# Kernel optimization log

Measured on AMD Instinct MI355X. Metric: run time of the kernel, lower is better.

Reference implementation:

```python
import jax, jax.numpy as jnp
import numpy as np

N, F, H, C = 50000, 128, 4, 32  # nodes, in-features, heads, per-head dim
E = 800000
D = H * C  # concat output dim = 128


def _tconv(x, src, dst, ea, Wq, bq, Wk, bk, Wv, bv, We, Ws, bs):
    # PyG TransformerConv (concat=True, root_weight=True, beta=False, eval mode)
    n = x.shape[0]
    q = (x @ Wq + bq).reshape(n, H, C)
    k = (x @ Wk + bk).reshape(n, H, C)
    v = (x @ Wv + bv).reshape(n, H, C)
    e = (ea @ We).reshape(-1, H, C)            # edge embedding [E,H,C]
    kj = k[src] + e                            # gathered keys + edge emb
    alpha = jnp.einsum('ehc,ehc->eh', q[dst], kj) / jnp.sqrt(jnp.float32(C))
    amax = jax.ops.segment_max(alpha, dst, num_segments=n)
    ex = jnp.exp(alpha - amax[dst])
    denom = jax.ops.segment_sum(ex, dst, num_segments=n)
    w = ex / (denom[dst] + 1e-16)              # segment softmax over in-edges
    msg = (v[src] + e) * w[:, :, None]
    out = jax.ops.segment_sum(msg, dst, num_segments=n).reshape(n, D)
    return out + x @ Ws + bs                   # skip connection


def setup_inputs() -> dict:
    key = jax.random.key(0)
    ks = jax.random.split(key, 24)
    s = lambda i, shape, scale: jax.random.normal(ks[i], shape, dtype=jnp.float32) * scale
    inp = {
        'x': s(0, (N, F), 1.0),
        'edge_index': jax.random.randint(ks[1], (2, E), 0, N),
        'edge_attr': s(2, (E,), 1.0),
        # layer 1 (in = F)
        'Wq1': s(3, (F, D), 1.0 / np.sqrt(F)), 'bq1': jnp.zeros((D,), jnp.float32),
        'Wk1': s(4, (F, D), 1.0 / np.sqrt(F)), 'bk1': jnp.zeros((D,), jnp.float32),
        'Wv1': s(5, (F, D), 1.0 / np.sqrt(F)), 'bv1': jnp.zeros((D,), jnp.float32),
        'We1': s(6, (1, D), 1.0),
        'Ws1': s(7, (F, D), 1.0 / np.sqrt(F)), 'bs1': jnp.zeros((D,), jnp.float32),
        # layer 2 (in = D)
        'Wq2': s(8, (D, D), 1.0 / np.sqrt(D)), 'bq2': jnp.zeros((D,), jnp.float32),
        'Wk2': s(9, (D, D), 1.0 / np.sqrt(D)), 'bk2': jnp.zeros((D,), jnp.float32),
        'Wv2': s(10, (D, D), 1.0 / np.sqrt(D)), 'bv2': jnp.zeros((D,), jnp.float32),
        'We2': s(11, (1, D), 1.0),
        'Ws2': s(12, (D, D), 1.0 / np.sqrt(D)), 'bs2': jnp.zeros((D,), jnp.float32),
    }
    return inp


def reference(x, edge_index, edge_attr,
              Wq1, bq1, Wk1, bk1, Wv1, bv1, We1, Ws1, bs1,
              Wq2, bq2, Wk2, bk2, Wv2, bv2, We2, Ws2, bs2):
    src, dst = edge_index[0], edge_index[1]
    ea = edge_attr.reshape(-1, 1)
    h = _tconv(x, src, dst, ea, Wq1, bq1, Wk1, bk1, Wv1, bv1, We1, Ws1, bs1)
    h = jax.nn.relu(h)  # dropout is identity in eval mode
    h = _tconv(h, src, dst, ea, Wq2, bq2, Wk2, bk2, Wv2, bv2, We2, Ws2, bs2)
    return jax.nn.relu(h)
```

## Files before the change

### kernel.cpp

```cpp
#include <hip/hip_runtime.h>


#define TPB 256

typedef __attribute__((ext_vector_type(8))) short short8v;
typedef __attribute__((ext_vector_type(4))) float f32x4;

__device__ __forceinline__ unsigned short f2bf(float f) {
    unsigned u = __float_as_uint(f);
    u = (u + 0x7FFFu + ((u >> 16) & 1u)) >> 16;
    return (unsigned short)u;
}
__device__ __forceinline__ float bf2f(unsigned short s) {
    return __uint_as_float((unsigned)s << 16);
}
__device__ __forceinline__ float4 bf4_to_f4(ushort4 u) {
    return make_float4(bf2f(u.x), bf2f(u.y), bf2f(u.z), bf2f(u.w));
}

__global__ void __launch_bounds__(TPB) cvt_bf16_k(const float* __restrict__ in,
                                                  unsigned short* __restrict__ out,
                                                  int n4)
{
    int i = blockIdx.x * TPB + threadIdx.x;
    if (i >= n4) return;
    float4 v = *(const float4*)(in + (size_t)i * 4);
    ushort4 o;
    o.x = f2bf(v.x); o.y = f2bf(v.y); o.z = f2bf(v.z); o.w = f2bf(v.w);
    *(ushort4*)(out + (size_t)i * 4) = o;
}

__global__ void __launch_bounds__(TPB) prepack_k(
    const float* __restrict__ Wq, const float* __restrict__ Wk,
    const float* __restrict__ Wv, const float* __restrict__ Ws,
    unsigned short* __restrict__ pack)
{
    int i = blockIdx.x * TPB + threadIdx.x;
    int j = i & 7, l = (i >> 3) & 63, t = (i >> 9) & 3, c = (i >> 11) & 7, g = (i >> 14) & 3;
    const float* W = g == 0 ? Wq : (g == 1 ? Wk : (g == 2 ? Wv : Ws));
    int kk = t * 32 + (l >> 4) * 8 + j;
    int nn = c * 16 + (l & 15);
    pack[i] = f2bf(W[kk * 128 + nn]);
}

__global__ void __launch_bounds__(TPB) gemm_mfma_k(
    const unsigned short* __restrict__ A, int M,
    const unsigned short* __restrict__ pack,
    const float* __restrict__ bq, const float* __restrict__ bk,
    const float* __restrict__ bv, const float* __restrict__ bs,
    unsigned short* __restrict__ oq, unsigned short* __restrict__ ok,
    unsigned short* __restrict__ ov, float* __restrict__ os)
{
    const int g = blockIdx.y;
    const int row0 = blockIdx.x * 128;
    const int wv = threadIdx.x >> 6;
    const int lane = threadIdx.x & 63;
    const int rbase = row0 + wv * 32;
    const int rlo = lane & 15;
    const int kg = (lane >> 4) * 8;

    const short8v z8 = {0, 0, 0, 0, 0, 0, 0, 0};
    short8v a[2][4];
#pragma unroll
    for (int m = 0; m < 2; ++m) {
        int row = rbase + m * 16 + rlo;
#pragma unroll
        for (int t = 0; t < 4; ++t)
            a[m][t] = (row < M) ? *(const short8v*)(A + (size_t)row * 128 + t * 32 + kg)
                                : z8;
    }

    f32x4 acc[2][8];
#pragma unroll
    for (int m = 0; m < 2; ++m)
#pragma unroll
        for (int c = 0; c < 8; ++c)
            acc[m][c] = (f32x4){0.f, 0.f, 0.f, 0.f};

    const unsigned short* bp = pack + (size_t)g * (8 * 4 * 512);
#pragma unroll
    for (int c = 0; c < 8; ++c) {
        short8v b[4];
#pragma unroll
        for (int t = 0; t < 4; ++t)
            b[t] = *(const short8v*)(bp + (c * 4 + t) * 512 + lane * 8);
#pragma unroll
        for (int t = 0; t < 4; ++t) {
            acc[0][c] = __builtin_amdgcn_mfma_f32_16x16x32_bf16(a[0][t], b[t], acc[0][c], 0, 0, 0);
            acc[1][c] = __builtin_amdgcn_mfma_f32_16x16x32_bf16(a[1][t], b[t], acc[1][c], 0, 0, 0);
        }
    }

    const float* bias = g == 0 ? bq : (g == 1 ? bk : (g == 2 ? bv : bs));
    const int rof = (lane >> 4) * 4;
    if (g == 3) {
#pragma unroll
        for (int c = 0; c < 8; ++c) {
            float bb = bias[c * 16 + rlo];
#pragma unroll
            for (int m = 0; m < 2; ++m)
#pragma unroll
                for (int j = 0; j < 4; ++j) {
                    int row = rbase + m * 16 + rof + j;
                    if (row < M) os[(size_t)row * 128 + c * 16 + rlo] = acc[m][c][j] + bb;
                }
        }
    } else {
        unsigned short* out = g == 0 ? oq : (g == 1 ? ok : ov);
#pragma unroll
        for (int c = 0; c < 8; ++c) {
            float bb = bias[c * 16 + rlo];
#pragma unroll
            for (int m = 0; m < 2; ++m)
#pragma unroll
                for (int j = 0; j < 4; ++j) {
                    int row = rbase + m * 16 + rof + j;
                    if (row < M) out[(size_t)row * 128 + c * 16 + rlo] = f2bf(acc[m][c][j] + bb);
                }
        }
    }
}

__global__ void __launch_bounds__(TPB) hist_k(const int* __restrict__ dst,
                                              int* __restrict__ deg, int E)
{
    int e = blockIdx.x * TPB + threadIdx.x;
    if (e < E) atomicAdd(&deg[dst[e]], 1);
}

__global__ void __launch_bounds__(TPB) scan_a_k(const int* __restrict__ deg, int n,
                                                int* __restrict__ incl,
                                                int* __restrict__ bsum)
{
    __shared__ int ts[TPB];
    const int base = blockIdx.x * 1024;
    int vals[4], s = 0;
#pragma unroll
    for (int j = 0; j < 4; ++j) {
        int i = base + threadIdx.x * 4 + j;
        vals[j] = (i < n) ? deg[i] : 0;
        s += vals[j];
    }
    ts[threadIdx.x] = s;
    __syncthreads();
    for (int off = 1; off < TPB; off <<= 1) {
        int u = (threadIdx.x >= off) ? ts[threadIdx.x - off] : 0;
        __syncthreads();
        ts[threadIdx.x] += u;
        __syncthreads();
    }
    int run = ts[threadIdx.x] - s;
#pragma unroll
    for (int j = 0; j < 4; ++j) {
        run += vals[j];
        int i = base + threadIdx.x * 4 + j;
        if (i < n) incl[i] = run;
    }
    if (threadIdx.x == TPB - 1) bsum[blockIdx.x] = ts[TPB - 1];
}

__global__ void __launch_bounds__(TPB) scan_b_k(int* __restrict__ bsum, int nb)
{
    __shared__ int ts[TPB];
    int t = threadIdx.x;
    int v = (t < nb) ? bsum[t] : 0;
    ts[t] = v;
    __syncthreads();
    for (int off = 1; off < TPB; off <<= 1) {
        int u = (t >= off) ? ts[t - off] : 0;
        __syncthreads();
        ts[t] += u;
        __syncthreads();
    }
    if (t < nb) bsum[t] = ts[t] - v;
}

__global__ void __launch_bounds__(TPB) finalize_k(const int* __restrict__ incl,
                                                  const int* __restrict__ deg,
                                                  const int* __restrict__ bsum, int n,
                                                  int* __restrict__ row_ptr,
                                                  int* __restrict__ cursor)
{
    const int base = blockIdx.x * 1024;
    const int boff = bsum[blockIdx.x];
#pragma unroll
    for (int j = 0; j < 4; ++j) {
        int i = base + threadIdx.x * 4 + j;
        if (i < n) {
            int iv = incl[i] + boff;
            int st = iv - deg[i];
            row_ptr[i] = st;
            cursor[i] = st;
            if (i == n - 1) row_ptr[n] = iv;
        }
    }
}

__global__ void __launch_bounds__(TPB) scatter_k(
    const int* __restrict__ src, const int* __restrict__ dst,
    const float* __restrict__ ea, int* __restrict__ cursor,
    int* __restrict__ csr_src, float* __restrict__ csr_ea, int E)
{
    int e = blockIdx.x * TPB + threadIdx.x;
    if (e >= E) return;
    int pos = atomicAdd(&cursor[dst[e]], 1);
    csr_src[pos] = src[e];
    csr_ea[pos] = ea[e];
}

template <bool BF16OUT>
__global__ void __launch_bounds__(TPB) node_attn_k(
    const unsigned short* __restrict__ q, const unsigned short* __restrict__ k,
    const unsigned short* __restrict__ v, const float* __restrict__ skip,
    const float* __restrict__ We,
    const int* __restrict__ row_ptr, const int* __restrict__ csr_src,
    const float* __restrict__ csr_ea,
    void* __restrict__ outp, int n)
{
    const int node = blockIdx.x * 4 + (threadIdx.x >> 6);
    if (node >= n) return;
    const int lane = threadIdx.x & 63;
    const bool vside = lane >= 32;
    const int c4 = (lane & 31) * 4;
    const unsigned short* gbase = vside ? v : k;

    const float4 we4 = *(const float4*)(We + c4);
    const float4 qv = bf4_to_f4(*(const ushort4*)(q + (size_t)node * 128 + c4));
    const int p0 = row_ptr[node], p1 = row_ptr[node + 1];
    const float C = 0.17677669529663687f;

    float m = -3.4e38f, l = 0.f;
    float4 acc = make_float4(0.f, 0.f, 0.f, 0.f);

    for (int base = p0; base < p1; base += 64) {
        const int cnt = min(64, p1 - base);
        int sv = 0;
        float av = 0.f;
        if (lane < cnt) {
            sv = csr_src[base + lane];
            av = csr_ea[base + lane];
        }
        int j = 0;
        for (; j + 4 <= cnt; j += 4) {
            int s0 = __shfl(sv, j), s1 = __shfl(sv, j + 1);
            int s2 = __shfl(sv, j + 2), s3 = __shfl(sv, j + 3);
            float a0 = __shfl(av, j), a1 = __shfl(av, j + 1);
            float a2 = __shfl(av, j + 2), a3 = __shfl(av, j + 3);
            ushort4 u0 = *(const ushort4*)(gbase + (size_t)s0 * 128 + c4);
            ushort4 u1 = *(const ushort4*)(gbase + (size_t)s1 * 128 + c4);
            ushort4 u2 = *(const ushort4*)(gbase + (size_t)s2 * 128 + c4);
            ushort4 u3 = *(const ushort4*)(gbase + (size_t)s3 * 128 + c4);
            float4 f0 = bf4_to_f4(u0), f1 = bf4_to_f4(u1);
            float4 f2 = bf4_to_f4(u2), f3 = bf4_to_f4(u3);
            float4 e0, e1, e2, e3;
            e0.x = fmaf(a0, we4.x, f0.x); e0.y = fmaf(a0, we4.y, f0.y);
            e0.z = fmaf(a0, we4.z, f0.z); e0.w = fmaf(a0, we4.w, f0.w);
            e1.x = fmaf(a1, we4.x, f1.x); e1.y = fmaf(a1, we4.y, f1.y);
            e1.z = fmaf(a1, we4.z, f1.z); e1.w = fmaf(a1, we4.w, f1.w);
            e2.x = fmaf(a2, we4.x, f2.x); e2.y = fmaf(a2, we4.y, f2.y);
            e2.z = fmaf(a2, we4.z, f2.z); e2.w = fmaf(a2, we4.w, f2.w);
            e3.x = fmaf(a3, we4.x, f3.x); e3.y = fmaf(a3, we4.y, f3.y);
            e3.z = fmaf(a3, we4.z, f3.z); e3.w = fmaf(a3, we4.w, f3.w);
            float d0 = e0.x * qv.x + e0.y * qv.y + e0.z * qv.z + e0.w * qv.w;
            float d1 = e1.x * qv.x + e1.y * qv.y + e1.z * qv.z + e1.w * qv.w;
            float d2 = e2.x * qv.x + e2.y * qv.y + e2.z * qv.z + e2.w * qv.w;
            float d3 = e3.x * qv.x + e3.y * qv.y + e3.z * qv.z + e3.w * qv.w;
            d0 += __shfl_xor(d0, 1); d0 += __shfl_xor(d0, 2); d0 += __shfl_xor(d0, 4);
            d1 += __shfl_xor(d1, 1); d1 += __shfl_xor(d1, 2); d1 += __shfl_xor(d1, 4);
            d2 += __shfl_xor(d2, 1); d2 += __shfl_xor(d2, 2); d2 += __shfl_xor(d2, 4);
            d3 += __shfl_xor(d3, 1); d3 += __shfl_xor(d3, 2); d3 += __shfl_xor(d3, 4);
            float al0 = __shfl(d0, lane & 31) * C;
            float al1 = __shfl(d1, lane & 31) * C;
            float al2 = __shfl(d2, lane & 31) * C;
            float al3 = __shfl(d3, lane & 31) * C;
            float mn = fmax(m, fmax(fmax(al0, al1), fmax(al2, al3)));
            float sc = __expf(m - mn);
            float pe0 = __expf(al0 - mn), pe1 = __expf(al1 - mn);
            float pe2 = __expf(al2 - mn), pe3 = __expf(al3 - mn);
            l = fmaf(l, sc, (pe0 + pe1) + (pe2 + pe3));
            acc.x = fmaf(acc.x, sc, fmaf(pe0, e0.x, fmaf(pe1, e1.x, fmaf(pe2, e2.x, pe3 * e3.x))));
            acc.y = fmaf(acc.y, sc, fmaf(pe0, e0.y, fmaf(pe1, e1.y, fmaf(pe2, e2.y, pe3 * e3.y))));
            acc.z = fmaf(acc.z, sc, fmaf(pe0, e0.z, fmaf(pe1, e1.z, fmaf(pe2, e2.z, pe3 * e3.z))));
            acc.w = fmaf(acc.w, sc, fmaf(pe0, e0.w, fmaf(pe1, e1.w, fmaf(pe2, e2.w, pe3 * e3.w))));
            m = mn;
        }
        for (; j < cnt; ++j) {
            int s0 = __shfl(sv, j);
            float a0 = __shfl(av, j);
            ushort4 u0 = *(const ushort4*)(gbase + (size_t)s0 * 128 + c4);
            float4 f0 = bf4_to_f4(u0);
            float4 e0;
            e0.x = fmaf(a0, we4.x, f0.x); e0.y = fmaf(a0, we4.y, f0.y);
            e0.z = fmaf(a0, we4.z, f0.z); e0.w = fmaf(a0, we4.w, f0.w);
            float d0 = e0.x * qv.x + e0.y * qv.y + e0.z * qv.z + e0.w * qv.w;
            d0 += __shfl_xor(d0, 1); d0 += __shfl_xor(d0, 2); d0 += __shfl_xor(d0, 4);
            float al0 = __shfl(d0, lane & 31) * C;
            float mn = fmax(m, al0);
            float sc = __expf(m - mn);
            float pe0 = __expf(al0 - mn);
            l = fmaf(l, sc, pe0);
            acc.x = fmaf(acc.x, sc, pe0 * e0.x);
            acc.y = fmaf(acc.y, sc, pe0 * e0.y);
            acc.z = fmaf(acc.z, sc, pe0 * e0.z);
            acc.w = fmaf(acc.w, sc, pe0 * e0.w);
            m = mn;
        }
    }

    if (vside) {
        float inv = 1.f / (l + 1e-16f);
        float4 sk = *(const float4*)(skip + (size_t)node * 128 + c4);
        float o0 = fmaxf(fmaf(acc.x, inv, sk.x), 0.f);
        float o1 = fmaxf(fmaf(acc.y, inv, sk.y), 0.f);
        float o2 = fmaxf(fmaf(acc.z, inv, sk.z), 0.f);
        float o3 = fmaxf(fmaf(acc.w, inv, sk.w), 0.f);
        if (BF16OUT) {
            ushort4 o;
            o.x = f2bf(o0); o.y = f2bf(o1); o.z = f2bf(o2); o.w = f2bf(o3);
            *(ushort4*)((unsigned short*)outp + (size_t)node * 128 + c4) = o;
        } else {
            *(float4*)((float*)outp + (size_t)node * 128 + c4) =
                make_float4(o0, o1, o2, o3);
        }
    }
}

extern "C" void kernel_launch(void* const* d_in, const int* in_sizes, int n_in,
                              void* d_out, int out_size, void* d_ws, size_t ws_size,
                              hipStream_t stream)
{
    const float* x   = (const float*)d_in[0];
    const int*   ei  = (const int*)d_in[1];
    const float* ea  = (const float*)d_in[2];
    const float* Wq1 = (const float*)d_in[3];  const float* bq1 = (const float*)d_in[4];
    const float* Wk1 = (const float*)d_in[5];  const float* bk1 = (const float*)d_in[6];
    const float* Wv1 = (const float*)d_in[7];  const float* bv1 = (const float*)d_in[8];
    const float* We1 = (const float*)d_in[9];
    const float* Ws1 = (const float*)d_in[10]; const float* bs1 = (const float*)d_in[11];
    const float* Wq2 = (const float*)d_in[12]; const float* bq2 = (const float*)d_in[13];
    const float* Wk2 = (const float*)d_in[14]; const float* bk2 = (const float*)d_in[15];
    const float* Wv2 = (const float*)d_in[16]; const float* bv2 = (const float*)d_in[17];
    const float* We2 = (const float*)d_in[18];
    const float* Ws2 = (const float*)d_in[19]; const float* bs2 = (const float*)d_in[20];

    const int N = in_sizes[0] / 128;
    const int E = in_sizes[1] / 2;
    const int* src = ei;
    const int* dst = ei + E;
    float* outf = (float*)d_out;

    unsigned short* q  = (unsigned short*)d_ws;
    unsigned short* k  = q + (size_t)N * 128;
    unsigned short* v  = k + (size_t)N * 128;
    float*          s  = (float*)(v + (size_t)N * 128);
    unsigned short* xb = (unsigned short*)(s + (size_t)N * 128);
    unsigned short* pk1 = xb + (size_t)N * 128;
    unsigned short* pk2 = pk1 + 65536;
    int*   row_ptr = (int*)(pk2 + 65536);
    int*   deg     = row_ptr + (N + 1);
    int*   incl    = deg + N;
    int*   cursor  = incl + N;
    int*   bsum    = cursor + N;
    int*   csr_src = bsum + 256;
    float* csr_ea  = (float*)(csr_src + E);

    const int gE   = (E + TPB - 1) / TPB;
    const int nb   = (N + 1023) / 1024;
    const int gN4  = (N + 3) / 4;
    const int gCv  = (N * 128 / 4 + TPB - 1) / TPB;
    const dim3 gG((N + 127) / 128, 4);

    hipMemsetAsync(deg, 0, (size_t)N * sizeof(int), stream);
    hist_k<<<gE, TPB, 0, stream>>>(dst, deg, E);
    scan_a_k<<<nb, TPB, 0, stream>>>(deg, N, incl, bsum);
    scan_b_k<<<1, TPB, 0, stream>>>(bsum, nb);
    finalize_k<<<nb, TPB, 0, stream>>>(incl, deg, bsum, N, row_ptr, cursor);
    scatter_k<<<gE, TPB, 0, stream>>>(src, dst, ea, cursor, csr_src, csr_ea, E);

    prepack_k<<<65536 / TPB, TPB, 0, stream>>>(Wq1, Wk1, Wv1, Ws1, pk1);
    prepack_k<<<65536 / TPB, TPB, 0, stream>>>(Wq2, Wk2, Wv2, Ws2, pk2);
    cvt_bf16_k<<<gCv, TPB, 0, stream>>>(x, xb, N * 128 / 4);

    gemm_mfma_k<<<gG, TPB, 0, stream>>>(xb, N, pk1, bq1, bk1, bv1, bs1, q, k, v, s);
    node_attn_k<true><<<gN4, TPB, 0, stream>>>(q, k, v, s, We1, row_ptr, csr_src,
                                               csr_ea, xb, N);
    gemm_mfma_k<<<gG, TPB, 0, stream>>>(xb, N, pk2, bq2, bk2, bv2, bs2, q, k, v, s);
    node_attn_k<false><<<gN4, TPB, 0, stream>>>(q, k, v, s, We2, row_ptr, csr_src,
                                                csr_ea, outf, N);
}
```

Before: 326.4 us.

## Factor edge embedding out of attention loop, use exp2, merge GEMM groups

The rank-1 edge embedding is pulled out of the per-edge inner loop. The score becomes q·k_src plus ea times a precomputed q·We, and the message sum adds sae·We once at the end. This removes per-edge FMAs. The softmax uses a raw v_exp_f32 (exp2) with the log2(e) scale folded into q, and gathers use 32-bit index arithmetic. The GEMM now loops over all four weight groups per block instead of using a 4-wide grid, and the two prepack launches are merged into one. This reuses A fragments but gives the GEMM a quarter as many blocks.

Result: slower. 340.0 us (+4.1%).

```diff
diff --git a/kernel.cpp b/kernel.cpp
--- a/kernel.cpp
+++ b/kernel.cpp
@@ -16,6 +16,11 @@
 }
 __device__ __forceinline__ float4 bf4_to_f4(ushort4 u) {
     return make_float4(bf2f(u.x), bf2f(u.y), bf2f(u.z), bf2f(u.w));
+}
+__device__ __forceinline__ float exp2_hw(float x) {
+    float r;
+    asm("v_exp_f32 %0, %1" : "=v"(r) : "v"(x));
+    return r;
 }
 
 __global__ void __launch_bounds__(TPB) cvt_bf16_k(const float* __restrict__ in,
@@ -31,13 +36,16 @@
 }
 
 __global__ void __launch_bounds__(TPB) prepack_k(
-    const float* __restrict__ Wq, const float* __restrict__ Wk,
-    const float* __restrict__ Wv, const float* __restrict__ Ws,
+    const float* __restrict__ Wq1, const float* __restrict__ Wk1,
+    const float* __restrict__ Wv1, const float* __restrict__ Ws1,
+    const float* __restrict__ Wq2, const float* __restrict__ Wk2,
+    const float* __restrict__ Wv2, const float* __restrict__ Ws2,
     unsigned short* __restrict__ pack)
 {
     int i = blockIdx.x * TPB + threadIdx.x;
-    int j = i & 7, l = (i >> 3) & 63, t = (i >> 9) & 3, c = (i >> 11) & 7, g = (i >> 14) & 3;
-    const float* W = g == 0 ? Wq : (g == 1 ? Wk : (g == 2 ? Wv : Ws));
+    int j = i & 7, l = (i >> 3) & 63, t = (i >> 9) & 3, c = (i >> 11) & 7, g = (i >> 14) & 7;
+    const float* Wt[8] = {Wq1, Wk1, Wv1, Ws1, Wq2, Wk2, Wv2, Ws2};
+    const float* W = Wt[g];
     int kk = t * 32 + (l >> 4) * 8 + j;
     int nn = c * 16 + (l & 15);
     pack[i] = f2bf(W[kk * 128 + nn]);
@@ -51,13 +59,13 @@
     unsigned short* __restrict__ oq, unsigned short* __restrict__ ok,
     unsigned short* __restrict__ ov, float* __restrict__ os)
 {
-    const int g = blockIdx.y;
     const int row0 = blockIdx.x * 128;
     const int wv = threadIdx.x >> 6;
     const int lane = threadIdx.x & 63;
     const int rbase = row0 + wv * 32;
     const int rlo = lane & 15;
     const int kg = (lane >> 4) * 8;
+    const int rof = (lane >> 4) * 4;
 
     const short8v z8 = {0, 0, 0, 0, 0, 0, 0, 0};
     short8v a[2][4];
@@ -70,53 +78,54 @@
                                 : z8;
     }
 
-    f32x4 acc[2][8];
-#pragma unroll
-    for (int m = 0; m < 2; ++m)
-#pragma unroll
-        for (int c = 0; c < 8; ++c)
-            acc[m][c] = (f32x4){0.f, 0.f, 0.f, 0.f};
-
-    const unsigned short* bp = pack + (size_t)g * (8 * 4 * 512);
-#pragma unroll
-    for (int c = 0; c < 8; ++c) {
-        short8v b[4];
-#pragma unroll
-        for (int t = 0; t < 4; ++t)
-            b[t] = *(const short8v*)(bp + (c * 4 + t) * 512 + lane * 8);
-#pragma unroll
-        for (int t = 0; t < 4; ++t) {
-            acc[0][c] = __builtin_amdgcn_mfma_f32_16x16x32_bf16(a[0][t], b[t], acc[0][c], 0, 0, 0);
-            acc[1][c] = __builtin_amdgcn_mfma_f32_16x16x32_bf16(a[1][t], b[t], acc[1][c], 0, 0, 0);
-        }
-    }
-
-    const float* bias = g == 0 ? bq : (g == 1 ? bk : (g == 2 ? bv : bs));
-    const int rof = (lane >> 4) * 4;
-    if (g == 3) {
+    for (int g = 0; g < 4; ++g) {
+        f32x4 acc[2][8];
+#pragma unroll
+        for (int m = 0; m < 2; ++m)
+#pragma unroll
+            for (int c = 0; c < 8; ++c)
+                acc[m][c] = (f32x4){0.f, 0.f, 0.f, 0.f};
+
+        const unsigned short* bp = pack + (size_t)g * (8 * 4 * 512);
 #pragma unroll
         for (int c = 0; c < 8; ++c) {
-            float bb = bias[c * 16 + rlo];
-#pragma unroll
-            for (int m = 0; m < 2; ++m)
-#pragma unroll
-                for (int j = 0; j < 4; ++j) {
-                    int row = rbase + m * 16 + rof + j;
-                    if (row < M) os[(size_t)row * 128 + c * 16 + rlo] = acc[m][c][j] + bb;
-                }
-        }
-    } else {
-        unsigned short* out = g == 0 ? oq : (g == 1 ? ok : ov);
-#pragma unroll
-        for (int c = 0; c < 8; ++c) {
-            float bb = bias[c * 16 + rlo];
-#pragma unroll
-            for (int m = 0; m < 2; ++m)
-#pragma unroll
-                for (int j = 0; j < 4; ++j) {
-                    int row = rbase + m * 16 + rof + j;
-                    if (row < M) out[(size_t)row * 128 + c * 16 + rlo] = f2bf(acc[m][c][j] + bb);
-                }
+            short8v b[4];
+#pragma unroll
+            for (int t = 0; t < 4; ++t)
+                b[t] = *(const short8v*)(bp + (c * 4 + t) * 512 + lane * 8);
+#pragma unroll
+            for (int t = 0; t < 4; ++t) {
+                acc[0][c] = __builtin_amdgcn_mfma_f32_16x16x32_bf16(a[0][t], b[t], acc[0][c], 0, 0, 0);
+                acc[1][c] = __builtin_amdgcn_mfma_f32_16x16x32_bf16(a[1][t], b[t], acc[1][c], 0, 0, 0);
+            }
+        }
+
+        const float* bias = g == 0 ? bq : (g == 1 ? bk : (g == 2 ? bv : bs));
+        if (g == 3) {
+#pragma unroll
+            for (int c = 0; c < 8; ++c) {
+                float bb = bias[c * 16 + rlo];
+#pragma unroll
+                for (int m = 0; m < 2; ++m)
+#pragma unroll
+                    for (int j = 0; j < 4; ++j) {
+                        int row = rbase + m * 16 + rof + j;
+                        if (row < M) os[(size_t)row * 128 + c * 16 + rlo] = acc[m][c][j] + bb;
+                    }
+            }
+        } else {
+            unsigned short* out = g == 0 ? oq : (g == 1 ? ok : ov);
+#pragma unroll
+            for (int c = 0; c < 8; ++c) {
+                float bb = bias[c * 16 + rlo];
+#pragma unroll
+                for (int m = 0; m < 2; ++m)
+#pragma unroll
+                    for (int j = 0; j < 4; ++j) {
+                        int row = rbase + m * 16 + rof + j;
+                        if (row < M) out[(size_t)row * 128 + c * 16 + rlo] = f2bf(acc[m][c][j] + bb);
+                    }
+            }
         }
     }
 }
@@ -224,12 +233,19 @@
     const int c4 = (lane & 31) * 4;
     const unsigned short* gbase = vside ? v : k;
 
+    const float C2 = 0.17677669529663687f * 1.44269504088896f;
     const float4 we4 = *(const float4*)(We + c4);
-    const float4 qv = bf4_to_f4(*(const ushort4*)(q + (size_t)node * 128 + c4));
+    float4 qv = bf4_to_f4(*(const ushort4*)(q + (size_t)node * 128 + c4));
+    qv.x *= C2; qv.y *= C2; qv.z *= C2; qv.w *= C2;
+
+    float qwe = qv.x * we4.x + qv.y * we4.y + qv.z * we4.z + qv.w * we4.w;
+    qwe += __shfl_xor(qwe, 1);
+    qwe += __shfl_xor(qwe, 2);
+    qwe += __shfl_xor(qwe, 4);
+
     const int p0 = row_ptr[node], p1 = row_ptr[node + 1];
-    const float C = 0.17677669529663687f;
-
-    float m = -3.4e38f, l = 0.f;
+
+    float m = -3.4e38f, l = 0.f, sae = 0.f;
     float4 acc = make_float4(0.f, 0.f, 0.f, 0.f);
 
     for (int base = p0; base < p1; base += 64) {
@@ -246,63 +262,53 @@
             int s2 = __shfl(sv, j + 2), s3 = __shfl(sv, j + 3);
             float a0 = __shfl(av, j), a1 = __shfl(av, j + 1);
             float a2 = __shfl(av, j + 2), a3 = __shfl(av, j + 3);
-            ushort4 u0 = *(const ushort4*)(gbase + (size_t)s0 * 128 + c4);
-            ushort4 u1 = *(const ushort4*)(gbase + (size_t)s1 * 128 + c4);
-            ushort4 u2 = *(const ushort4*)(gbase + (size_t)s2 * 128 + c4);
-            ushort4 u3 = *(const ushort4*)(gbase + (size_t)s3 * 128 + c4);
+            ushort4 u0 = *(const ushort4*)(gbase + (unsigned)s0 * 128u + c4);
+            ushort4 u1 = *(const ushort4*)(gbase + (unsigned)s1 * 128u + c4);
+            ushort4 u2 = *(const ushort4*)(gbase + (unsigned)s2 * 128u + c4);
+            ushort4 u3 = *(const ushort4*)(gbase + (unsigned)s3 * 128u + c4);
             float4 f0 = bf4_to_f4(u0), f1 = bf4_to_f4(u1);
             float4 f2 = bf4_to_f4(u2), f3 = bf4_to_f4(u3);
-            float4 e0, e1, e2, e3;
-            e0.x = fmaf(a0, we4.x, f0.x); e0.y = fmaf(a0, we4.y, f0.y);
-            e0.z = fmaf(a0, we4.z, f0.z); e0.w = fmaf(a0, we4.w, f0.w);
-            e1.x = fmaf(a1, we4.x, f1.x); e1.y = fmaf(a1, we4.y, f1.y);
-            e1.z = fmaf(a1, we4.z, f1.z); e1.w = fmaf(a1, we4.w, f1.w);
-            e2.x = fmaf(a2, we4.x, f2.x); e2.y = fmaf(a2, we4.y, f2.y);
-            e2.z = fmaf(a2, we4.z, f2.z); e2.w = fmaf(a2, we4.w, f2.w);
-            e3.x = fmaf(a3, we4.x, f3.x); e3.y = fmaf(a3, we4.y, f3.y);
-            e3.z = fmaf(a3, we4.z, f3.z); e3.w = fmaf(a3, we4.w, f3.w);
-            float d0 = e0.x * qv.x + e0.y * qv.y + e0.z * qv.z + e0.w * qv.w;
-            float d1 = e1.x * qv.x + e1.y * qv.y + e1.z * qv.z + e1.w * qv.w;
-            float d2 = e2.x * qv.x + e2.y * qv.y + e2.z * qv.z + e2.w * qv.w;
-            float d3 = e3.x * qv.x + e3.y * qv.y + e3.z * qv.z + e3.w * qv.w;
+            float d0 = f0.x * qv.x + f0.y * qv.y + f0.z * qv.z + f0.w * qv.w;
+            float d1 = f1.x * qv.x + f1.y * qv.y + f1.z * qv.z + f1.w * qv.w;
+            float d2 = f2.x * qv.x + f2.y * qv.y + f2.z * qv.z + f2.w * qv.w;
+            float d3 = f3.x * qv.x + f3.y * qv.y + f3.z * qv.z + f3.w * qv.w;
             d0 += __shfl_xor(d0, 1); d0 += __shfl_xor(d0, 2); d0 += __shfl_xor(d0, 4);
             d1 += __shfl_xor(d1, 1); d1 += __shfl_xor(d1, 2); d1 += __shfl_xor(d1, 4);
             d2 += __shfl_xor(d2, 1); d2 += __shfl_xor(d2, 2); d2 += __shfl_xor(d2, 4);
             d3 += __shfl_xor(d3, 1); d3 += __shfl_xor(d3, 2); d3 += __shfl_xor(d3, 4);
-            float al0 = __shfl(d0, lane & 31) * C;
-            float al1 = __shfl(d1, lane & 31) * C;
-            float al2 = __shfl(d2, lane & 31) * C;
-            float al3 = __shfl(d3, lane & 31) * C;
-            float mn = fmax(m, fmax(fmax(al0, al1), fmax(al2, al3)));
-            float sc = __expf(m - mn);
-            float pe0 = __expf(al0 - mn), pe1 = __expf(al1 - mn);
-            float pe2 = __expf(al2 - mn), pe3 = __expf(al3 - mn);
+            float al0 = fmaf(a0, qwe, __shfl(d0, lane & 31));
+            float al1 = fmaf(a1, qwe, __shfl(d1, lane & 31));
+            float al2 = fmaf(a2, qwe, __shfl(d2, lane & 31));
+            float al3 = fmaf(a3, qwe, __shfl(d3, lane & 31));
+            float mn = fmaxf(m, fmaxf(fmaxf(al0, al1), fmaxf(al2, al3)));
+            float sc = exp2_hw(m - mn);
+            float pe0 = exp2_hw(al0 - mn), pe1 = exp2_hw(al1 - mn);
+            float pe2 = exp2_hw(al2 - mn), pe3 = exp2_hw(al3 - mn);
             l = fmaf(l, sc, (pe0 + pe1) + (pe2 + pe3));
-            acc.x = fmaf(acc.x, sc, fmaf(pe0, e0.x, fmaf(pe1, e1.x, fmaf(pe2, e2.x, pe3 * e3.x))));
-            acc.y = fmaf(acc.y, sc, fmaf(pe0, e0.y, fmaf(pe1, e1.y, fmaf(pe2, e2.y, pe3 * e3.y))));
-            acc.z = fmaf(acc.z, sc, fmaf(pe0, e0.z, fmaf(pe1, e1.z, fmaf(pe2, e2.z, pe3 * e3.z))));
-            acc.w = fmaf(acc.w, sc, fmaf(pe0, e0.w, fmaf(pe1, e1.w, fmaf(pe2, e2.w, pe3 * e3.w))));
+            sae = fmaf(sae, sc, fmaf(pe3, a3, fmaf(pe2, a2, fmaf(pe1, a1, pe0 * a0))));
+            acc.x = fmaf(acc.x, sc, fmaf(pe0, f0.x, fmaf(pe1, f1.x, fmaf(pe2, f2.x, pe3 * f3.x))));
+            acc.y = fmaf(acc.y, sc, fmaf(pe0, f0.y, fmaf(pe1, f1.y, fmaf(pe2, f2.y, pe3 * f3.y))));
+            acc.z = fmaf(acc.z, sc, fmaf(pe0, f0.z, fmaf(pe1, f1.z, fmaf(pe2, f2.z, pe3 * f3.z))));
+            acc.w = fmaf(acc.w, sc, fmaf(pe0, f0.w, fmaf(pe1, f1.w, fmaf(pe2, f2.w, pe3 * f3.w))));
             m = mn;
         }
         for (; j < cnt; ++j) {
             int s0 = __shfl(sv, j);
             float a0 = __shfl(av, j);
-            ushort4 u0 = *(const ushort4*)(gbase + (size_t)s0 * 128 + c4);
+            ushort4 u0 = *(const ushort4*)(gbase + (unsigned)s0 * 128u + c4);
             float4 f0 = bf4_to_f4(u0);
-            float4 e0;
-            e0.x = fmaf(a0, we4.x, f0.x); e0.y = fmaf(a0, we4.y, f0.y);
-            e0.z = fmaf(a0, we4.z, f0.z); e0.w = fmaf(a0, we4.w, f0.w);
-            float d0 = e0.x * qv.x + e0.y * qv.y + e0.z * qv.z + e0.w * qv.w;
+            float d0 = f0.x * qv.x + f0.y * qv.y + f0.z * qv.z + f0.w * qv.w;
             d0 += __shfl_xor(d0, 1); d0 += __shfl_xor(d0, 2); d0 += __shfl_xor(d0, 4);
-            float al0 = __shfl(d0, lane & 31) * C;
-            float mn = fmax(m, al0);
-            float sc = __expf(m - mn);
-            float pe0 = __expf(al0 - mn);
+            float al0 = fmaf(a0, qwe, __shfl(d0, lane & 31));
+            float mn = fmaxf(m, al0);
+            float sc = exp2_hw(m - mn);
+            float pe0 = exp2_hw(al0 - mn);
             l = fmaf(l, sc, pe0);
-            acc.x = fmaf(acc.x, sc, pe0 * e0.x);
-            acc.y = fmaf(acc.y, sc, pe0 * e0.y);
-            acc.z = fmaf(acc.z, sc, pe0 * e0.z);
-            acc.w = fmaf(acc.w, sc, pe0 * e0.w);
+            sae = fmaf(sae, sc, pe0 * a0);
+            acc.x = fmaf(acc.x, sc, pe0 * f0.x);
+            acc.y = fmaf(acc.y, sc, pe0 * f0.y);
+            acc.z = fmaf(acc.z, sc, pe0 * f0.z);
+            acc.w = fmaf(acc.w, sc, pe0 * f0.w);
             m = mn;
         }
     }
@@ -310,10 +316,10 @@
     if (vside) {
         float inv = 1.f / (l + 1e-16f);
         float4 sk = *(const float4*)(skip + (size_t)node * 128 + c4);
-        float o0 = fmaxf(fmaf(acc.x, inv, sk.x), 0.f);
-        float o1 = fmaxf(fmaf(acc.y, inv, sk.y), 0.f);
-        float o2 = fmaxf(fmaf(acc.z, inv, sk.z), 0.f);
-        float o3 = fmaxf(fmaf(acc.w, inv, sk.w), 0.f);
+        float o0 = fmaxf(fmaf(fmaf(sae, we4.x, acc.x), inv, sk.x), 0.f);
+        float o1 = fmaxf(fmaf(fmaf(sae, we4.y, acc.y), inv, sk.y), 0.f);
+        float o2 = fmaxf(fmaf(fmaf(sae, we4.z, acc.z), inv, sk.z), 0.f);
+        float o3 = fmaxf(fmaf(fmaf(sae, we4.w, acc.w), inv, sk.w), 0.f);
         if (BF16OUT) {
             ushort4 o;
             o.x = f2bf(o0); o.y = f2bf(o1); o.z = f2bf(o2); o.w = f2bf(o3);
@@ -354,9 +360,8 @@
     unsigned short* v  = k + (size_t)N * 128;
     float*          s  = (float*)(v + (size_t)N * 128);
     unsigned short* xb = (unsigned short*)(s + (size_t)N * 128);
-    unsigned short* pk1 = xb + (size_t)N * 128;
-    unsigned short* pk2 = pk1 + 65536;
-    int*   row_ptr = (int*)(pk2 + 65536);
+    unsigned short* pk = xb + (size_t)N * 128;
+    int*   row_ptr = (int*)(pk + 131072);
     int*   deg     = row_ptr + (N + 1);
     int*   incl    = deg + N;
     int*   cursor  = incl + N;
@@ -368,7 +373,7 @@
     const int nb   = (N + 1023) / 1024;
     const int gN4  = (N + 3) / 4;
     const int gCv  = (N * 128 / 4 + TPB - 1) / TPB;
-    const dim3 gG((N + 127) / 128, 4);
+    const int gG   = (N + 127) / 128;
 
     hipMemsetAsync(deg, 0, (size_t)N * sizeof(int), stream);
     hist_k<<<gE, TPB, 0, stream>>>(dst, deg, E);
@@ -377,14 +382,15 @@
     finalize_k<<<nb, TPB, 0, stream>>>(incl, deg, bsum, N, row_ptr, cursor);
     scatter_k<<<gE, TPB, 0, stream>>>(src, dst, ea, cursor, csr_src, csr_ea, E);
 
-    prepack_k<<<65536 / TPB, TPB, 0, stream>>>(Wq1, Wk1, Wv1, Ws1, pk1);
-    prepack_k<<<65536 / TPB, TPB, 0, stream>>>(Wq2, Wk2, Wv2, Ws2, pk2);
+    prepack_k<<<131072 / TPB, TPB, 0, stream>>>(Wq1, Wk1, Wv1, Ws1,
+                                                Wq2, Wk2, Wv2, Ws2, pk);
     cvt_bf16_k<<<gCv, TPB, 0, stream>>>(x, xb, N * 128 / 4);
 
-    gemm_mfma_k<<<gG, TPB, 0, stream>>>(xb, N, pk1, bq1, bk1, bv1, bs1, q, k, v, s);
+    gemm_mfma_k<<<gG, TPB, 0, stream>>>(xb, N, pk, bq1, bk1, bv1, bs1, q, k, v, s);
     node_attn_k<true><<<gN4, TPB, 0, stream>>>(q, k, v, s, We1, row_ptr, csr_src,
                                                csr_ea, xb, N);
-    gemm_mfma_k<<<gG, TPB, 0, stream>>>(xb, N, pk2, bq2, bk2, bv2, bs2, q, k, v, s);
+    gemm_mfma_k<<<gG, TPB, 0, stream>>>(xb, N, pk + 65536, bq2, bk2, bv2, bs2,
+                                        q, k, v, s);
     node_attn_k<false><<<gN4, TPB, 0, stream>>>(q, k, v, s, We2, row_ptr, csr_src,
                                                 csr_ea, outf, N);
 }
```
